# Kernel optimization log

Hardware: AMD Instinct MI355X
Metric: run time of the kernel (lower is better)

The kernel has to match this reference:

```python
import jax, jax.numpy as jnp
import numpy as np

P = 1024
H, W = 160, 160
TANFOVX = 0.5
TANFOVY = 0.5
SCALE_MODIFIER = 1.0


def _quat_to_rot(q):
    # q: [P,4] normalized quaternions (r, x, y, z)
    r, x, y, z = q[:, 0], q[:, 1], q[:, 2], q[:, 3]
    row0 = jnp.stack([1 - 2 * (y * y + z * z), 2 * (x * y - r * z), 2 * (x * z + r * y)], -1)
    row1 = jnp.stack([2 * (x * y + r * z), 1 - 2 * (x * x + z * z), 2 * (y * z - r * x)], -1)
    row2 = jnp.stack([2 * (x * z - r * y), 2 * (y * z + r * x), 1 - 2 * (x * x + y * y)], -1)
    return jnp.stack([row0, row1, row2], -2)  # [P,3,3]


def _rasterize(means3D, colors_precomp, opacities, scales, rotations, bg, viewmatrix, projmatrix):
    fx = W / (2.0 * TANFOVX)
    fy = H / (2.0 * TANFOVY)

    hom = jnp.concatenate([means3D, jnp.ones((means3D.shape[0], 1), means3D.dtype)], -1)  # [P,4]
    t = hom @ viewmatrix.T  # view space [P,4]
    tz = t[:, 2]
    depth_ok = tz > 0.2  # near-plane cull as in CUDA kernel

    p_hom = hom @ projmatrix.T
    p_w = 1.0 / (p_hom[:, 3] + 1e-7)
    p_proj = p_hom[:, :3] * p_w[:, None]
    # ndc2pix
    px = ((p_proj[:, 0] + 1.0) * W - 1.0) * 0.5
    py = ((p_proj[:, 1] + 1.0) * H - 1.0) * 0.5

    # 3D covariance: Sigma = R S S^T R^T
    s = scales * SCALE_MODIFIER
    R = _quat_to_rot(rotations)
    M = R * s[:, None, :]  # R @ diag(s)
    cov3D = M @ jnp.swapaxes(M, 1, 2)  # [P,3,3]

    # EWA projection to 2D covariance
    limx = 1.3 * TANFOVX
    limy = 1.3 * TANFOVY
    txz = jnp.clip(t[:, 0] / tz, -limx, limx) * tz
    tyz = jnp.clip(t[:, 1] / tz, -limy, limy) * tz
    zero = jnp.zeros_like(tz)
    J = jnp.stack([
        jnp.stack([fx / tz, zero, -fx * txz / (tz * tz)], -1),
        jnp.stack([zero, fy / tz, -fy * tyz / (tz * tz)], -1),
    ], -2)  # [P,2,3]
    Wm = viewmatrix[:3, :3]
    T = jnp.einsum('pij,jk->pik', J, Wm)  # [P,2,3]
    cov2 = jnp.einsum('pij,pjk,plk->pil', T, cov3D, T)  # [P,2,2]
    a = cov2[:, 0, 0] + 0.3  # low-pass filter on diagonal
    c = cov2[:, 1, 1] + 0.3
    b = cov2[:, 0, 1]
    det = a * c - b * b
    det_ok = det > 0
    inv_det = jnp.where(det_ok, 1.0 / jnp.where(det_ok, det, 1.0), 0.0)
    conic_a = c * inv_det
    conic_b = -b * inv_det
    conic_c = a * inv_det

    mid = 0.5 * (a + c)
    lam1 = mid + jnp.sqrt(jnp.maximum(0.1, mid * mid - det))
    radius = jnp.ceil(3.0 * jnp.sqrt(lam1))

    valid = depth_ok & det_ok
    radii = jnp.where(valid, radius, 0.0).astype(jnp.int32)

    # per-pixel Gaussian evaluation
    ys, xs = jnp.meshgrid(jnp.arange(H, dtype=means3D.dtype), jnp.arange(W, dtype=means3D.dtype), indexing='ij')
    dx = px[:, None, None] - xs[None]  # [P,H,W]
    dy = py[:, None, None] - ys[None]
    power = (-0.5 * (conic_a[:, None, None] * dx * dx + conic_c[:, None, None] * dy * dy)
             - conic_b[:, None, None] * dx * dy)
    op = opacities[:, 0][:, None, None]
    alpha = jnp.minimum(0.99, op * jnp.exp(power))
    alpha = jnp.where((power > 0.0) | (alpha < 1.0 / 255.0) | (~valid)[:, None, None], 0.0, alpha)

    # front-to-back alpha compositing in depth order
    depth_key = jnp.where(valid, tz, jnp.inf)
    order = jnp.argsort(depth_key)
    alpha_s = alpha[order]            # [P,H,W]
    colors_s = colors_precomp[order]  # [P,3]
    Tcum = jnp.cumprod(1.0 - alpha_s, axis=0)
    Texcl = jnp.concatenate([jnp.ones((1, H, W), alpha_s.dtype), Tcum[:-1]], 0)
    w = alpha_s * Texcl
    color = jnp.einsum('phw,pc->chw', w, colors_s) + Tcum[-1][None] * bg[:, None, None]
    return color, radii


def setup_inputs() -> dict:
    key = jax.random.key(0)
    ks = jax.random.split(key, 6)
    u = jax.random.uniform(ks[0], (P, 3), dtype=jnp.float32)
    means3D = jnp.stack([u[:, 0] * 4 - 2, u[:, 1] * 4 - 2, u[:, 2] * 6 + 2], -1)  # inside frustum
    means2D = jnp.zeros((P, 3), jnp.float32)  # gradient-holder only, unused in fwd
    colors_precomp = jax.random.uniform(ks[1], (P, 3), dtype=jnp.float32)
    opacities = jax.random.uniform(ks[2], (P, 1), dtype=jnp.float32) * 0.9 + 0.05
    scales = jax.random.uniform(ks[3], (P, 3), dtype=jnp.float32) * 0.15 + 0.05
    q = jax.random.normal(ks[4], (P, 4), dtype=jnp.float32)
    rotations = q / jnp.linalg.norm(q, axis=-1, keepdims=True)
    bg = jnp.zeros((3,), jnp.float32)
    viewmatrix = jnp.eye(4, dtype=jnp.float32)
    znear, zfar = 0.01, 100.0
    persp = jnp.array([[1.0 / TANFOVX, 0, 0, 0],
                       [0, 1.0 / TANFOVY, 0, 0],
                       [0, 0, zfar / (zfar - znear), -zfar * znear / (zfar - znear)],
                       [0, 0, 1.0, 0]], dtype=jnp.float32)
    projmatrix = persp @ viewmatrix
    campos = jnp.zeros((3,), jnp.float32)
    return dict(means3D=means3D, means2D=means2D, colors_precomp=colors_precomp,
                opacities=opacities, scales=scales, rotations=rotations,
                bg=bg, viewmatrix=viewmatrix, projmatrix=projmatrix, campos=campos)


def reference(means3D, means2D, colors_precomp, opacities, scales, rotations, bg, viewmatrix, projmatrix, campos):
    color, radii = _rasterize(means3D, colors_precomp, opacities, scales, rotations, bg, viewmatrix, projmatrix)
    return color, radii
```

## Files before the change

kernel.cpp:

```cpp
#include <hip/hip_runtime.h>
#include <math.h>

#define PCNT 1024
#define HH 160
#define WW 160
#define NPIX (HH * WW)
#define TILE 8
#define TX (WW / TILE)
#define TY (HH / TILE)
#define NTILES (TX * TY)
#define NBLK 256

__global__ __launch_bounds__(512) void k_all(
    const float* __restrict__ means, const float* __restrict__ cols,
    const float* __restrict__ ops, const float* __restrict__ scales,
    const float* __restrict__ rots, const float* __restrict__ vm,
    const float* __restrict__ pm, const float* __restrict__ bg,
    float* __restrict__ out)
{
    __shared__ float4 spA[PCNT];
    __shared__ float4 spB[PCNT];
    __shared__ float  spC[PCNT];
    __shared__ float4 cl[PCNT];
    __shared__ unsigned int kbits[PCNT];
    __shared__ __align__(16) unsigned long long sl[2][PCNT];
    __shared__ unsigned short ranked[2][PCNT];
    __shared__ float4 part[8][64];
    __shared__ unsigned long long masks[2][16];
    __shared__ int offs[2][16];
    __shared__ int sn[2];

    int tid = threadIdx.x;
    int bid = blockIdx.x;
    int wave = tid >> 6, lane = tid & 63;

    bool two = (bid + NBLK) < NTILES;
    int gsz   = two ? 4 : 8;
    int group = two ? (wave >> 2) : 0;
    int gwave = two ? (wave & 3) : wave;
    int gtid  = tid - group * (gsz << 6);
    int cpw   = 16 / gsz;

    const float HL2E = 0.72134752044448170f;
    const float L2E  = 1.4426950408889634f;
    const float LN2  = 0.69314718055994531f;

    for (int i = tid; i < PCNT; i += 512) {
        float mx = means[3 * i], my = means[3 * i + 1], mz = means[3 * i + 2];

        float t0 = vm[0] * mx + vm[1] * my + vm[2] * mz + vm[3];
        float t1 = vm[4] * mx + vm[5] * my + vm[6] * mz + vm[7];
        float t2 = vm[8] * mx + vm[9] * my + vm[10] * mz + vm[11];
        bool depth_ok = t2 > 0.2f;

        float ph0 = pm[0] * mx + pm[1] * my + pm[2] * mz + pm[3];
        float ph1 = pm[4] * mx + pm[5] * my + pm[6] * mz + pm[7];
        float ph3 = pm[12] * mx + pm[13] * my + pm[14] * mz + pm[15];
        float pw = 1.0f / (ph3 + 1e-7f);
        float px = ((ph0 * pw + 1.0f) * (float)WW - 1.0f) * 0.5f;
        float py = ((ph1 * pw + 1.0f) * (float)HH - 1.0f) * 0.5f;

        float4 q = *(const float4*)(rots + 4 * i);
        float qr = q.x, qx = q.y, qy = q.z, qz = q.w;
        float R00 = 1.f - 2.f * (qy * qy + qz * qz), R01 = 2.f * (qx * qy - qr * qz), R02 = 2.f * (qx * qz + qr * qy);
        float R10 = 2.f * (qx * qy + qr * qz), R11 = 1.f - 2.f * (qx * qx + qz * qz), R12 = 2.f * (qy * qz - qr * qx);
        float R20 = 2.f * (qx * qz - qr * qy), R21 = 2.f * (qy * qz + qr * qx), R22 = 1.f - 2.f * (qx * qx + qy * qy);

        float s0 = scales[3 * i], s1 = scales[3 * i + 1], s2 = scales[3 * i + 2];
        float M00 = R00 * s0, M01 = R01 * s1, M02 = R02 * s2;
        float M10 = R10 * s0, M11 = R11 * s1, M12 = R12 * s2;
        float M20 = R20 * s0, M21 = R21 * s1, M22 = R22 * s2;
        float c00 = M00 * M00 + M01 * M01 + M02 * M02;
        float c01 = M00 * M10 + M01 * M11 + M02 * M12;
        float c02 = M00 * M20 + M01 * M21 + M02 * M22;
        float c11 = M10 * M10 + M11 * M11 + M12 * M12;
        float c12 = M10 * M20 + M11 * M21 + M12 * M22;
        float c22 = M20 * M20 + M21 * M21 + M22 * M22;

        const float fx = 160.0f, fy = 160.0f;
        const float limx = 0.65f, limy = 0.65f;
        float txz = fminf(limx, fmaxf(-limx, t0 / t2)) * t2;
        float tyz = fminf(limy, fmaxf(-limy, t1 / t2)) * t2;
        float rz = 1.0f / t2;
        float J00 = fx * rz, J02 = -fx * txz * rz * rz;
        float J11 = fy * rz, J12 = -fy * tyz * rz * rz;

        float T00 = J00 * vm[0] + J02 * vm[8];
        float T01 = J00 * vm[1] + J02 * vm[9];
        float T02 = J00 * vm[2] + J02 * vm[10];
        float T10 = J11 * vm[4] + J12 * vm[8];
        float T11 = J11 * vm[5] + J12 * vm[9];
        float T12 = J11 * vm[6] + J12 * vm[10];

        float u00 = T00 * c00 + T01 * c01 + T02 * c02;
        float u01 = T00 * c01 + T01 * c11 + T02 * c12;
        float u02 = T00 * c02 + T01 * c12 + T02 * c22;
        float u10 = T10 * c00 + T11 * c01 + T12 * c02;
        float u11 = T10 * c01 + T11 * c11 + T12 * c12;
        float u12 = T10 * c02 + T11 * c12 + T12 * c22;
        float a  = u00 * T00 + u01 * T01 + u02 * T02 + 0.3f;
        float bb = u00 * T10 + u01 * T11 + u02 * T12;
        float cc = u10 * T10 + u11 * T11 + u12 * T12 + 0.3f;

        float det = a * cc - bb * bb;
        bool det_ok = det > 0.0f;
        float inv_det = det_ok ? 1.0f / det : 0.0f;
        float conA = cc * inv_det, conB = -bb * inv_det, conC = a * inv_det;
        float mid = 0.5f * (a + cc);
        float lam1 = mid + sqrtf(fmaxf(0.1f, mid * mid - det));
        float radius = ceilf(3.0f * sqrtf(lam1));
        bool valid = depth_ok && det_ok;

        if (bid == 0)
            out[3 * NPIX + i] = valid ? (float)(int)radius : 0.0f;

        if (valid) {
            float op = ops[i];
            float l2; asm("v_log_f32 %0, %1" : "=v"(l2) : "v"(255.0f * op));
            float tau = fmaxf(fmaf(l2, LN2, 0.02f), 0.0f);
            float hx = sqrtf(2.0f * tau * a);
            float hy = sqrtf(2.0f * tau * cc);
            spA[i] = make_float4(px, py, conA * HL2E, conB * L2E);
            spB[i] = make_float4(conC * HL2E, op, cols[3 * i], cols[3 * i + 1]);
            spC[i] = cols[3 * i + 2];
            cl[i] = make_float4(px, py, hx, hy);
            kbits[i] = __float_as_uint(t2);
        } else {
            spA[i] = make_float4(0.f, 0.f, 0.f, 0.f);
            spB[i] = make_float4(0.f, 0.f, 0.f, 0.f);
            spC[i] = 0.f;
            cl[i] = make_float4(0.f, 0.f, -1e9f, -1e9f);
            kbits[i] = 0x7f800000u;
        }
    }
    __syncthreads();

    int tile = bid + group * NBLK;
    int tx = tile % TX, ty = tile / TX;
    float x0 = (float)(tx * TILE), y0 = (float)(ty * TILE);

    for (int k = 0; k < cpw; ++k) {
        int c = gwave * cpw + k;
        float4 cv = cl[c * 64 + lane];
        bool ov = (cv.x + cv.z >= x0) & (cv.x - cv.z <= x0 + (float)(TILE - 1)) &
                  (cv.y + cv.w >= y0) & (cv.y - cv.w <= y0 + (float)(TILE - 1));
        unsigned long long m = __ballot(ov);
        if (lane == 0) masks[group][c] = m;
    }
    __syncthreads();
    if (gtid == 0) {
        int acc = 0;
        #pragma unroll
        for (int c = 0; c < 16; ++c) { offs[group][c] = acc; acc += __popcll(masks[group][c]); }
        sn[group] = acc;
    }
    __syncthreads();
    for (int k = 0; k < cpw; ++k) {
        int c = gwave * cpw + k;
        unsigned long long m = masks[group][c];
        if ((m >> lane) & 1ull) {
            int g = c * 64 + lane;
            int pos = offs[group][c] + __popcll(m & ((1ull << lane) - 1ull));
            sl[group][pos] = ((unsigned long long)kbits[g] << 32) | (unsigned int)g;
        }
    }
    __syncthreads();
    int n = sn[group];
    for (int t = n + gtid; t < ((n + 3) & ~3) && t < PCNT; t += 64 * gsz)
        sl[group][t] = ~0ull;
    __syncthreads();

    for (int t = gtid; t < n; t += 64 * gsz) {
        unsigned long long key = sl[group][t];
        int cnt = 0;
        const unsigned long long* base = sl[group];
        for (int k = 0; k < n; k += 4) {
            ulonglong2 p0 = *(const ulonglong2*)(base + k);
            ulonglong2 p1 = *(const ulonglong2*)(base + k + 2);
            cnt += (p0.x < key) ? 1 : 0;
            cnt += (p0.y < key) ? 1 : 0;
            cnt += (p1.x < key) ? 1 : 0;
            cnt += (p1.y < key) ? 1 : 0;
        }
        ranked[group][cnt] = (unsigned short)(key & 1023u);
    }
    __syncthreads();

    float fxp = x0 + (float)(lane & 7);
    float fyp = y0 + (float)(lane >> 3);

    float T = 1.0f, C0 = 0.f, C1 = 0.f, C2 = 0.f;
    int per = (n + gsz - 1) / gsz;
    int lo = gwave * per, hi = min(n, lo + per);
    int i = lo;
    for (; i + 4 <= hi; i += 4) {
        int id0 = ranked[group][i + 0];
        int id1 = ranked[group][i + 1];
        int id2 = ranked[group][i + 2];
        int id3 = ranked[group][i + 3];
        float4 A0 = spA[id0], B0 = spB[id0];
        float4 A1 = spA[id1], B1 = spB[id1];
        float4 A2 = spA[id2], B2 = spB[id2];
        float4 A3 = spA[id3], B3 = spB[id3];
        float cb0 = spC[id0], cb1 = spC[id1], cb2 = spC[id2], cb3 = spC[id3];

        float dx0 = A0.x - fxp, dy0 = A0.y - fyp;
        float dx1 = A1.x - fxp, dy1 = A1.y - fyp;
        float dx2 = A2.x - fxp, dy2 = A2.y - fyp;
        float dx3 = A3.x - fxp, dy3 = A3.y - fyp;
        float p0 = -(A0.z * dx0 * dx0 + B0.x * dy0 * dy0) - A0.w * dx0 * dy0;
        float p1 = -(A1.z * dx1 * dx1 + B1.x * dy1 * dy1) - A1.w * dx1 * dy1;
        float p2 = -(A2.z * dx2 * dx2 + B2.x * dy2 * dy2) - A2.w * dx2 * dy2;
        float p3 = -(A3.z * dx3 * dx3 + B3.x * dy3 * dy3) - A3.w * dx3 * dy3;
        float e0, e1, e2, e3;
        asm("v_exp_f32 %0, %1" : "=v"(e0) : "v"(p0));
        asm("v_exp_f32 %0, %1" : "=v"(e1) : "v"(p1));
        asm("v_exp_f32 %0, %1" : "=v"(e2) : "v"(p2));
        asm("v_exp_f32 %0, %1" : "=v"(e3) : "v"(p3));
        float al0 = fminf(0.99f, B0.y * e0); if (p0 > 0.0f || al0 < (1.0f / 255.0f)) al0 = 0.0f;
        float al1 = fminf(0.99f, B1.y * e1); if (p1 > 0.0f || al1 < (1.0f / 255.0f)) al1 = 0.0f;
        float al2 = fminf(0.99f, B2.y * e2); if (p2 > 0.0f || al2 < (1.0f / 255.0f)) al2 = 0.0f;
        float al3 = fminf(0.99f, B3.y * e3); if (p3 > 0.0f || al3 < (1.0f / 255.0f)) al3 = 0.0f;

        float w;
        w = al0 * T; C0 = fmaf(w, B0.z, C0); C1 = fmaf(w, B0.w, C1); C2 = fmaf(w, cb0, C2); T *= (1.0f - al0);
        w = al1 * T; C0 = fmaf(w, B1.z, C0); C1 = fmaf(w, B1.w, C1); C2 = fmaf(w, cb1, C2); T *= (1.0f - al1);
        w = al2 * T; C0 = fmaf(w, B2.z, C0); C1 = fmaf(w, B2.w, C1); C2 = fmaf(w, cb2, C2); T *= (1.0f - al2);
        w = al3 * T; C0 = fmaf(w, B3.z, C0); C1 = fmaf(w, B3.w, C1); C2 = fmaf(w, cb3, C2); T *= (1.0f - al3);
    }
    for (; i < hi; ++i) {
        int id = ranked[group][i];
        float4 v0 = spA[id];
        float4 v1 = spB[id];
        float cbv = spC[id];
        float dx = v0.x - fxp, dy = v0.y - fyp;
        float p = -(v0.z * dx * dx + v1.x * dy * dy) - v0.w * dx * dy;
        float e; asm("v_exp_f32 %0, %1" : "=v"(e) : "v"(p));
        float al = fminf(0.99f, v1.y * e);
        if (p > 0.0f || al < (1.0f / 255.0f)) al = 0.0f;
        float w = al * T;
        C0 = fmaf(w, v1.z, C0);
        C1 = fmaf(w, v1.w, C1);
        C2 = fmaf(w, cbv, C2);
        T *= (1.0f - al);
    }

    part[wave][lane] = make_float4(C0, C1, C2, T);
    __syncthreads();

    if (gtid < 64) {
        float Tt = 1.0f, c0 = 0.f, c1 = 0.f, c2 = 0.f;
        int sbase = group * gsz;
        for (int s = 0; s < gsz; ++s) {
            float4 v = part[sbase + s][gtid];
            c0 = fmaf(Tt, v.x, c0);
            c1 = fmaf(Tt, v.y, c1);
            c2 = fmaf(Tt, v.z, c2);
            Tt *= v.w;
        }
        int pix = (ty * TILE + (gtid >> 3)) * WW + tx * TILE + (gtid & 7);
        out[pix]            = c0 + Tt * bg[0];
        out[NPIX + pix]     = c1 + Tt * bg[1];
        out[2 * NPIX + pix] = c2 + Tt * bg[2];
    }
}

extern "C" void kernel_launch(void* const* d_in, const int* in_sizes, int n_in,
                              void* d_out, int out_size, void* d_ws, size_t ws_size,
                              hipStream_t stream) {
    const float* means  = (const float*)d_in[0];
    const float* cols   = (const float*)d_in[2];
    const float* ops    = (const float*)d_in[3];
    const float* scales = (const float*)d_in[4];
    const float* rots   = (const float*)d_in[5];
    const float* bg     = (const float*)d_in[6];
    const float* vm     = (const float*)d_in[7];
    const float* pm     = (const float*)d_in[8];

    float* out = (float*)d_out;

    k_all<<<NBLK, 512, 0, stream>>>(means, cols, ops, scales, rots, vm, pm, bg, out);
}
```

Baseline: 14.42 us.

## Cull gaussians per tile by exact conic minimum instead of bounding box

Tile culling now finds the minimum of the gaussian's quadratic form over the tile rectangle, checking the four edges plus the case where the center lies inside. It compares that minimum against a log-opacity threshold instead of testing an axis-aligned extent box. Fewer gaussians should pass per tile, so less sorting and blending work follows. The per-wave split is also rounded to multiples of four so rank indices can be read as one ushort4 vector load. The cull costs more arithmetic per gaussian, and the changed threshold constant could alter which contributions are kept.

```diff
diff --git a/kernel.cpp b/kernel.cpp
--- a/kernel.cpp
+++ b/kernel.cpp
@@ -24,7 +24,7 @@
     __shared__ float4 cl[PCNT];
     __shared__ unsigned int kbits[PCNT];
     __shared__ __align__(16) unsigned long long sl[2][PCNT];
-    __shared__ unsigned short ranked[2][PCNT];
+    __shared__ __align__(16) unsigned short ranked[2][PCNT];
     __shared__ float4 part[8][64];
     __shared__ unsigned long long masks[2][16];
     __shared__ int offs[2][16];
@@ -43,7 +43,6 @@
 
     const float HL2E = 0.72134752044448170f;
     const float L2E  = 1.4426950408889634f;
-    const float LN2  = 0.69314718055994531f;
 
     for (int i = tid; i < PCNT; i += 512) {
         float mx = means[3 * i], my = means[3 * i + 1], mz = means[3 * i + 2];
@@ -117,19 +116,17 @@
         if (valid) {
             float op = ops[i];
             float l2; asm("v_log_f32 %0, %1" : "=v"(l2) : "v"(255.0f * op));
-            float tau = fmaxf(fmaf(l2, LN2, 0.02f), 0.0f);
-            float hx = sqrtf(2.0f * tau * a);
-            float hy = sqrtf(2.0f * tau * cc);
+            float tau2 = fmaxf(l2 + 0.05f, 0.0f);
             spA[i] = make_float4(px, py, conA * HL2E, conB * L2E);
             spB[i] = make_float4(conC * HL2E, op, cols[3 * i], cols[3 * i + 1]);
             spC[i] = cols[3 * i + 2];
-            cl[i] = make_float4(px, py, hx, hy);
+            cl[i] = make_float4(px, py, tau2, 0.f);
             kbits[i] = __float_as_uint(t2);
         } else {
             spA[i] = make_float4(0.f, 0.f, 0.f, 0.f);
             spB[i] = make_float4(0.f, 0.f, 0.f, 0.f);
             spC[i] = 0.f;
-            cl[i] = make_float4(0.f, 0.f, -1e9f, -1e9f);
+            cl[i] = make_float4(0.f, 0.f, -1e30f, 0.f);
             kbits[i] = 0x7f800000u;
         }
     }
@@ -141,11 +138,30 @@
 
     for (int k = 0; k < cpw; ++k) {
         int c = gwave * cpw + k;
-        float4 cv = cl[c * 64 + lane];
-        bool ov = (cv.x + cv.z >= x0) & (cv.x - cv.z <= x0 + (float)(TILE - 1)) &
-                  (cv.y + cv.w >= y0) & (cv.y - cv.w <= y0 + (float)(TILE - 1));
-        unsigned long long m = __ballot(ov);
-        if (lane == 0) masks[group][c] = m;
+        int g = c * 64 + lane;
+        float4 cv = cl[g];
+        float alf = spA[g].z;
+        float bet = spA[g].w;
+        float gam = spB[g].x;
+        float dxl = x0 - cv.x, dxh = x0 + 7.0f - cv.x;
+        float dyl = y0 - cv.y, dyh = y0 + 7.0f - cv.y;
+
+        float t0e = fminf(fmaxf(-bet * dxl / (2.0f * gam), dyl), dyh);
+        float q0 = alf * dxl * dxl + bet * dxl * t0e + gam * t0e * t0e;
+        float t1e = fminf(fmaxf(-bet * dxh / (2.0f * gam), dyl), dyh);
+        float q1 = alf * dxh * dxh + bet * dxh * t1e + gam * t1e * t1e;
+        float t2e = fminf(fmaxf(-bet * dyl / (2.0f * alf), dxl), dxh);
+        float q2 = alf * t2e * t2e + bet * t2e * dyl + gam * dyl * dyl;
+        float t3e = fminf(fmaxf(-bet * dyh / (2.0f * alf), dxl), dxh);
+        float q3 = alf * t3e * t3e + bet * t3e * dyh + gam * dyh * dyh;
+
+        bool inside = (dxl <= 0.0f) & (dxh >= 0.0f) & (dyl <= 0.0f) & (dyh >= 0.0f);
+        float m = fminf(fminf(q0, q1), fminf(q2, q3));
+        if (inside) m = 0.0f;
+        bool ov = (m <= cv.z);
+
+        unsigned long long mk = __ballot(ov);
+        if (lane == 0) masks[group][c] = mk;
     }
     __syncthreads();
     if (gtid == 0) {
@@ -191,13 +207,13 @@
 
     float T = 1.0f, C0 = 0.f, C1 = 0.f, C2 = 0.f;
     int per = (n + gsz - 1) / gsz;
-    int lo = gwave * per, hi = min(n, lo + per);
+    per = (per + 3) & ~3;
+    int lo = gwave * per; if (lo > n) lo = n;
+    int hi = min(n, lo + per);
     int i = lo;
     for (; i + 4 <= hi; i += 4) {
-        int id0 = ranked[group][i + 0];
-        int id1 = ranked[group][i + 1];
-        int id2 = ranked[group][i + 2];
-        int id3 = ranked[group][i + 3];
+        ushort4 ids = *(const ushort4*)(&ranked[group][i]);
+        int id0 = ids.x, id1 = ids.y, id2 = ids.z, id3 = ids.w;
         float4 A0 = spA[id0], B0 = spB[id0];
         float4 A1 = spA[id1], B1 = spB[id1];
         float4 A2 = spA[id2], B2 = spB[id2];
```

Measured after the change: 14.89 us. 3.3% more time.
